# Performance work log

Measured on AMD Instinct MI355X. Metric: run time of the kernel, lower is better.

Reference implementation:

```python
import jax, jax.numpy as jnp
import numpy as np

L = 2048          # seq len
DIM = 1024        # model dim
NL = 12           # num layers
VOCAB = 50257
PAD_VOCAB = 50264 # vocab padded to multiple of 8 for embedding
N = 16            # ssm state dim
K = 4             # conv kernel size
E = 2048          # d_inner = expand * dim
DTR = 64          # dt_rank = ceil(dim/16)
EPS = 1e-5


def setup_inputs() -> dict:
    key = jax.random.key(0)
    ks = jax.random.split(key, 12)
    s = 0.02
    f32 = jnp.float32
    # HiPPO-style A init: A_log = log(1..N) broadcast over channels
    A_log = jnp.log(jnp.broadcast_to(jnp.arange(1, N + 1, dtype=f32), (NL, E, N)))
    return {
        "input_ids": jax.random.randint(ks[0], (L,), 0, VOCAB),
        "embed": jax.random.normal(ks[1], (PAD_VOCAB, DIM), f32) * s,
        "in_proj_w": jax.random.normal(ks[2], (NL, 2 * E, DIM), f32) * s,
        "conv_w": jax.random.normal(ks[3], (NL, E, K), f32) * s,
        "conv_b": jnp.zeros((NL, E), f32),
        "x_proj_w": jax.random.normal(ks[4], (NL, DTR + 2 * N, E), f32) * s,
        "dt_proj_w": jax.random.normal(ks[5], (NL, E, DTR), f32) * s,
        "dt_proj_b": jax.random.normal(ks[6], (NL, E), f32) * 0.1,
        "A_log": A_log,
        "D_param": jnp.ones((NL, E), f32),
        "out_proj_w": jax.random.normal(ks[7], (NL, DIM, E), f32) * s,
        "norm_w": jnp.ones((NL, DIM), f32),
        "norm_f_w": jnp.ones((DIM,), f32),
        "head_w": jax.random.normal(ks[8], (VOCAB, DIM), f32) * s,
    }


def rmsnorm(x, w):
    # per-token RMSNorm over last axis (matches eqx.nn.RMSNorm vmapped per token)
    inv = jax.lax.rsqrt(jnp.mean(x * x, axis=-1, keepdims=True) + EPS)
    return x * inv * w


def causal_dw_conv(x, w, b):
    # x: [L, E], w: [E, K] depthwise causal conv, b: [E]
    out = jax.lax.conv_general_dilated(
        x.T[None],            # [1, E, L]
        w[:, None, :],        # [E, 1, K]
        (1,), [(K - 1, 0)],
        feature_group_count=E,
        dimension_numbers=("NCH", "OIH", "NCH"),
    )
    return out[0].T + b       # [L, E]


def mamba_block(x, in_w, cw, cb, xp_w, dt_w, dt_b, A_log, D, out_w):
    # x: [L, DIM]
    xz = x @ in_w.T                       # [L, 2E]
    xi, z = xz[:, :E], xz[:, E:]
    xc = jax.nn.silu(causal_dw_conv(xi, cw, cb))   # [L, E]
    dbc = xc @ xp_w.T                     # [L, DTR + 2N]
    dt = jax.nn.softplus(dbc[:, :DTR] @ dt_w.T + dt_b)  # [L, E]
    B = dbc[:, DTR:DTR + N]               # [L, N]
    C = dbc[:, DTR + N:]                  # [L, N]
    A = -jnp.exp(A_log)                   # [E, N]
    dA = jnp.exp(dt[:, :, None] * A)                       # [L, E, N]
    dBu = dt[:, :, None] * B[:, None, :] * xc[:, :, None]  # [L, E, N]

    def step(h, inp):
        dA_t, dBu_t = inp
        h = dA_t * h + dBu_t
        return h, h

    _, hs = jax.lax.scan(step, jnp.zeros((E, N), x.dtype), (dA, dBu))
    y = jnp.einsum("len,ln->le", hs, C) + D * xc
    y = y * jax.nn.silu(z)
    return y @ out_w.T                    # [L, DIM]


def reference(input_ids, embed, in_proj_w, conv_w, conv_b, x_proj_w,
              dt_proj_w, dt_proj_b, A_log, D_param, out_proj_w,
              norm_w, norm_f_w, head_w):
    x = embed[input_ids]                  # [L, DIM]
    res = None
    for i in range(NL):
        res = x + res if res is not None else x
        h = rmsnorm(res, norm_w[i])
        x = mamba_block(h, in_proj_w[i], conv_w[i], conv_b[i], x_proj_w[i],
                        dt_proj_w[i], dt_proj_b[i], A_log[i], D_param[i],
                        out_proj_w[i])
    res = x + res
    x = rmsnorm(res, norm_f_w)
    return x @ head_w.T                   # [L, VOCAB]
```

## Files before the change

kernel.cpp:

```cpp
#include <hip/hip_runtime.h>
#include <math.h>

#define LSEQ 2048
#define DMODEL 1024
#define NLAYER 12
#define NVOCAB 50257
#define NPADV 50432
#define EDIM 2048
#define NST 16
#define DTRANK 64
#define EPSV 1e-5f
#define NCHUNK 64
#define TCHUNK 32

typedef __attribute__((ext_vector_type(4))) float float4v;
typedef __attribute__((ext_vector_type(8))) short short8v;
typedef __attribute__((ext_vector_type(4))) unsigned short ushort4v;
typedef unsigned short u16;

__device__ __forceinline__ u16 f2bf(float f) {
    union { float f; unsigned int u; } v; v.f = f;
    unsigned int r = v.u + 0x7FFFu + ((v.u >> 16) & 1u);
    return (u16)(r >> 16);
}

__device__ __forceinline__ ushort4v cvt4(float4 a) {
    ushort4v r; r[0] = f2bf(a.x); r[1] = f2bf(a.y); r[2] = f2bf(a.z); r[3] = f2bf(a.w);
    return r;
}

__device__ __forceinline__ short8v pack8(float4 a, float4 b) {
    short8v r;
    r[0] = (short)f2bf(a.x); r[1] = (short)f2bf(a.y); r[2] = (short)f2bf(a.z); r[3] = (short)f2bf(a.w);
    r[4] = (short)f2bf(b.x); r[5] = (short)f2bf(b.y); r[6] = (short)f2bf(b.z); r[7] = (short)f2bf(b.w);
    return r;
}

__device__ __forceinline__ float4v mfma_bf16(short8v a, short8v b, float4v c) {
    return __builtin_amdgcn_mfma_f32_16x16x32_bf16(a, b, c, 0, 0, 0);
}

__device__ __forceinline__ void gload_lds16(const void* g, void* l) {
    __builtin_amdgcn_global_load_lds(
        (const __attribute__((address_space(1))) unsigned int*)g,
        (__attribute__((address_space(3))) unsigned int*)l,
        16, 0, 0);
}

__global__ __launch_bounds__(256) void k_embed(const int* __restrict__ ids,
                                               const float* __restrict__ emb,
                                               float* __restrict__ res) {
    const int t = blockIdx.x;
    const int row = ids[t];
    ((float4*)(res + (size_t)t * DMODEL))[threadIdx.x] =
        ((const float4*)(emb + (size_t)row * DMODEL))[threadIdx.x];
}

template<bool ADD>
__global__ __launch_bounds__(256) void k_addnorm(float* __restrict__ res,
                                                 const float* __restrict__ xin,
                                                 const float* __restrict__ w,
                                                 u16* __restrict__ h) {
    const int t = blockIdx.x;
    const int i = threadIdx.x;
    float4 r = ((float4*)(res + (size_t)t * DMODEL))[i];
    if (ADD) {
        float4 xv = ((const float4*)(xin + (size_t)t * DMODEL))[i];
        r.x += xv.x; r.y += xv.y; r.z += xv.z; r.w += xv.w;
        ((float4*)(res + (size_t)t * DMODEL))[i] = r;
    }
    float ss = r.x * r.x + r.y * r.y + r.z * r.z + r.w * r.w;
#pragma unroll
    for (int off = 32; off > 0; off >>= 1) ss += __shfl_xor(ss, off);
    __shared__ float part[4];
    if ((i & 63) == 0) part[i >> 6] = ss;
    __syncthreads();
    float tot = part[0] + part[1] + part[2] + part[3];
    const float inv = rsqrtf(tot * (1.f / DMODEL) + EPSV);
    float4 wv = ((const float4*)w)[i];
    float4 o;
    o.x = r.x * inv * wv.x; o.y = r.y * inv * wv.y;
    o.z = r.z * inv * wv.z; o.w = r.w * inv * wv.w;
    ((ushort4v*)(h + (size_t)t * DMODEL))[i] = cvt4(o);
}

__global__ __launch_bounds__(256) void k_cvt(const float* __restrict__ s, u16* __restrict__ d,
                                             long long n, long long ntot) {
    const long long stride = (long long)gridDim.x * 256 * 8;
    for (long long i = ((long long)blockIdx.x * 256 + threadIdx.x) * 8; i < ntot; i += stride) {
        ushort4v lo, hi;
        if (i < n) {
            float4 a = *(const float4*)(s + i);
            float4 b = *(const float4*)(s + i + 4);
            lo = cvt4(a); hi = cvt4(b);
        } else {
            lo[0] = lo[1] = lo[2] = lo[3] = 0;
            hi[0] = hi[1] = hi[2] = hi[3] = 0;
        }
        *(ushort4v*)(d + i) = lo;
        *(ushort4v*)(d + i + 4) = hi;
    }
}

__global__ __launch_bounds__(256) void k_cvt2(const float* __restrict__ sa, u16* __restrict__ da, long long na,
                                              const float* __restrict__ sb, u16* __restrict__ db, long long nb) {
    const long long tot = na + nb;
    const long long stride = (long long)gridDim.x * 256 * 8;
    for (long long i = ((long long)blockIdx.x * 256 + threadIdx.x) * 8; i < tot; i += stride) {
        const float* s; u16* d; long long o;
        if (i < na) { s = sa; d = da; o = i; } else { s = sb; d = db; o = i - na; }
        float4 a = *(const float4*)(s + o);
        float4 b = *(const float4*)(s + o + 4);
        *(ushort4v*)(d + o) = cvt4(a);
        *(ushort4v*)(d + o + 4) = cvt4(b);
    }
}

template<int MT>
__global__ __launch_bounds__(512, 2) void k_gemm256(const u16* __restrict__ A,
                                                    const u16* __restrict__ W,
                                                    float* __restrict__ C,
                                                    int N, int K, int ldc, int cpx) {
    __shared__ __align__(128) u16 lds[2][2][2][8192];
    const int tid = threadIdx.x;
    const int w = tid >> 6;
    const int lane = tid & 63;
    const int l16 = lane & 15;
    const int quad = lane >> 4;
    const int wm = (w >> 2) * 128;
    const int wn = (w & 3) * 64;
    const int ha = w >> 2;
    const int hb = (w >> 1) & 1;
    const int bid = blockIdx.x;
    const int orig = (bid & 7) * cpx + (bid >> 3);
    const int bm = orig & (MT - 1);
    const int bn = orig / MT;
    const int row0 = bm * 256, col0 = bn * 256;

    int srow[2], scol[2];
#pragma unroll
    for (int q = 0; q < 2; ++q) {
        int off = q * 8192 + w * 1024 + lane * 16;
        off ^= ((off >> 7) & 7) << 4;
        srow[q] = off >> 7;
        scol[q] = (off & 127) >> 1;
    }
    const int qx0 = (quad * 16) ^ ((l16 & 7) << 4);
    const int bA0 = l16 * 128 + qx0;
    const int bA1 = bA0 ^ 64;
    const int bB0 = ((wn & 127) + l16) * 128 + qx0;
    const int bB1 = bB0 ^ 64;

    float4v acc[8][4];
#pragma unroll
    for (int i = 0; i < 8; ++i)
#pragma unroll
        for (int j = 0; j < 4; ++j)
#pragma unroll
            for (int r = 0; r < 4; ++r) acc[i][j][r] = 0.f;

    const int NT = K >> 6;

    auto stage_tile = [&](int buf, int t) {
#pragma unroll
        for (int h = 0; h < 2; ++h)
#pragma unroll
            for (int q = 0; q < 2; ++q) {
                gload_lds16(A + (size_t)(row0 + h * 128 + srow[q]) * K + t * 64 + scol[q],
                            &lds[buf][0][h][q * 4096 + w * 512]);
                gload_lds16(W + (size_t)(col0 + h * 128 + srow[q]) * K + t * 64 + scol[q],
                            &lds[buf][1][h][q * 4096 + w * 512]);
            }
    };

    stage_tile(0, 0);
    stage_tile(1, 1);
    asm volatile("s_waitcnt vmcnt(8)" ::: "memory");
    __builtin_amdgcn_s_barrier();

    for (int n = 0; n < NT; ++n) {
        const u16* As0 = &lds[n & 1][0][ha][0];
        const u16* Bs0 = &lds[n & 1][1][hb][0];
#pragma unroll
        for (int ph = 0; ph < 4; ++ph) {
            const int ih = ph & 1;
            const int ks = ph >> 1;
            const int bA = ks ? bA1 : bA0;
            const int bB = ks ? bB1 : bB0;
            short8v af[4], bf[4];
#pragma unroll
            for (int ii = 0; ii < 4; ++ii)
                af[ii] = *(const short8v*)((const char*)As0 + (bA + ih * 8192 + ii * 2048));
#pragma unroll
            for (int j = 0; j < 4; ++j)
                bf[j] = *(const short8v*)((const char*)Bs0 + (bB + j * 2048));
            __builtin_amdgcn_s_barrier();
            __builtin_amdgcn_s_setprio(1);
#pragma unroll
            for (int ii = 0; ii < 4; ++ii)
#pragma unroll
                for (int j = 0; j < 4; ++j)
                    acc[ih * 4 + ii][j] = mfma_bf16(af[ii], bf[j], acc[ih * 4 + ii][j]);
            __builtin_amdgcn_s_setprio(0);
            if (ph == 3) {
                if (n + 2 < NT) {
                    stage_tile(n & 1, n + 2);
                    asm volatile("s_waitcnt vmcnt(8)" ::: "memory");
                } else if (n < NT - 1) {
                    asm volatile("s_waitcnt vmcnt(0)" ::: "memory");
                }
            }
            __builtin_amdgcn_s_barrier();
        }
    }

#pragma unroll
    for (int i = 0; i < 8; ++i) {
        const int row = row0 + wm + i * 16 + quad * 4;
#pragma unroll
        for (int j = 0; j < 4; ++j) {
            const int col = col0 + wn + j * 16 + l16;
            if (col < N) {
#pragma unroll
                for (int r = 0; r < 4; ++r)
                    C[(size_t)(row + r) * ldc + col] = acc[i][j][r];
            }
        }
    }
}

template<int TM, int TN>
__global__ __launch_bounds__(256) void k_gemm_bf(const u16* __restrict__ A,
                                                 const u16* __restrict__ W,
                                                 float* __restrict__ C,
                                                 int N, int K, int ldc) {
    constexpr int NI = TM / 32, NJ = TN / 32, CA = TM / 64, CB = TN / 64;
    __shared__ u16 As[TM * 32];
    __shared__ u16 Bs[TN * 32];
    const int tid = threadIdx.x;
    const int lane = tid & 63;
    const int wave = tid >> 6;
    const int l16 = lane & 15;
    const int quad = lane >> 4;
    const int wm = (wave >> 1) * (TM / 2);
    const int wn = (wave & 1) * (TN / 2);
    const int srow = lane >> 2;
    const int scol = (((lane & 3) ^ ((lane >> 2) & 3))) * 8;
    const int bm = blockIdx.x, bn = blockIdx.y;

    const u16* Ab = A + ((size_t)bm * TM + srow) * K + scol;
    const u16* Wb = W + ((size_t)bn * TN + srow) * K + scol;

    const int qs = (quad ^ (l16 & 3)) * 8;

    float4v acc[NI][NJ];
#pragma unroll
    for (int i = 0; i < NI; ++i)
#pragma unroll
        for (int j = 0; j < NJ; ++j)
#pragma unroll
            for (int r = 0; r < 4; ++r) acc[i][j][r] = 0.f;

    for (int k0 = 0; k0 < K; k0 += 32) {
#pragma unroll
        for (int c = 0; c < CA; ++c) {
            const int chunk = wave * CA + c;
            gload_lds16(Ab + (size_t)chunk * 16 * K + k0, &As[chunk * 512]);
        }
#pragma unroll
        for (int c = 0; c < CB; ++c) {
            const int chunk = wave * CB + c;
            gload_lds16(Wb + (size_t)chunk * 16 * K + k0, &Bs[chunk * 512]);
        }
        __syncthreads();
        short8v af[NI], bfr[NJ];
#pragma unroll
        for (int i = 0; i < NI; ++i)
            af[i] = *(const short8v*)&As[(wm + i * 16 + l16) * 32 + qs];
#pragma unroll
        for (int j = 0; j < NJ; ++j)
            bfr[j] = *(const short8v*)&Bs[(wn + j * 16 + l16) * 32 + qs];
#pragma unroll
        for (int i = 0; i < NI; ++i)
#pragma unroll
            for (int j = 0; j < NJ; ++j)
                acc[i][j] = mfma_bf16(af[i], bfr[j], acc[i][j]);
        __syncthreads();
    }

#pragma unroll
    for (int i = 0; i < NI; ++i) {
        const int row0 = bm * TM + wm + i * 16 + quad * 4;
#pragma unroll
        for (int j = 0; j < NJ; ++j) {
            const int col = bn * TN + wn + j * 16 + l16;
            if (col < N) {
#pragma unroll
                for (int r = 0; r < 4; ++r)
                    C[(size_t)(row0 + r) * ldc + col] = acc[i][j][r];
            }
        }
    }
}

template<int EPI>
__global__ __launch_bounds__(256) void k_gemm(const float* __restrict__ A,
                                              const float* __restrict__ W,
                                              float* __restrict__ C,
                                              const float* __restrict__ bias,
                                              int N, int K, int lda, int ldw, int ldc) {
    __shared__ u16 As[128][32];
    __shared__ u16 Bs[128][32];
    const int tid = threadIdx.x;
    const int lane = tid & 63;
    const int wave = tid >> 6;
    const int l16 = lane & 15;
    const int quad = lane >> 4;
    const int wm = (wave >> 1) * 64;
    const int wn = (wave & 1) * 64;
    const int srow = tid >> 3;
    const int scol = (tid & 7) * 4;
    const int bm = blockIdx.x, bn = blockIdx.y;

    const float* Ap = A + (size_t)(bm * 128 + srow) * lda + scol;
    const int gn0 = bn * 128 + srow;

    float4 apf[4], bpf[4];
#pragma unroll
    for (int i = 0; i < 4; ++i) {
        apf[i] = *(const float4*)(Ap + (size_t)(32 * i) * lda);
        const int gn = gn0 + 32 * i;
        bpf[i] = (gn < N) ? *(const float4*)(W + (size_t)gn * ldw + scol)
                          : make_float4(0.f, 0.f, 0.f, 0.f);
    }

    float4v acc[4][4];
#pragma unroll
    for (int i = 0; i < 4; ++i)
#pragma unroll
        for (int j = 0; j < 4; ++j)
#pragma unroll
            for (int r = 0; r < 4; ++r) acc[i][j][r] = 0.f;

    int k0 = 0;
    while (true) {
#pragma unroll
        for (int i = 0; i < 4; ++i) {
            *(ushort4v*)&As[srow + 32 * i][scol] = cvt4(apf[i]);
            *(ushort4v*)&Bs[srow + 32 * i][scol] = cvt4(bpf[i]);
        }
        __syncthreads();
        k0 += 32;
        const bool more = (k0 < K);
        if (more) {
#pragma unroll
            for (int i = 0; i < 4; ++i) {
                apf[i] = *(const float4*)(Ap + (size_t)(32 * i) * lda + k0);
                const int gn = gn0 + 32 * i;
                bpf[i] = (gn < N) ? *(const float4*)(W + (size_t)gn * ldw + scol + k0)
                                  : make_float4(0.f, 0.f, 0.f, 0.f);
            }
        }
        short8v af[4], bfr[4];
#pragma unroll
        for (int i = 0; i < 4; ++i)
            af[i] = *(const short8v*)&As[wm + i * 16 + l16][quad * 8];
#pragma unroll
        for (int j = 0; j < 4; ++j)
            bfr[j] = *(const short8v*)&Bs[wn + j * 16 + l16][quad * 8];
#pragma unroll
        for (int i = 0; i < 4; ++i)
#pragma unroll
            for (int j = 0; j < 4; ++j)
                acc[i][j] = mfma_bf16(af[i], bfr[j], acc[i][j]);
        if (!more) break;
        __syncthreads();
    }

#pragma unroll
    for (int i = 0; i < 4; ++i) {
        const int row0 = bm * 128 + wm + i * 16 + quad * 4;
#pragma unroll
        for (int j = 0; j < 4; ++j) {
            const int col = bn * 128 + wn + j * 16 + l16;
            if (col < N) {
#pragma unroll
                for (int r = 0; r < 4; ++r) {
                    float v = acc[i][j][r];
                    if (EPI == 1) {
                        v += bias[col];
                        v = (v > 20.f) ? v : log1pf(__expf(v));
                    }
                    C[(size_t)(row0 + r) * ldc + col] = v;
                }
            }
        }
    }
}

__global__ __launch_bounds__(256) void k_conv(const float* __restrict__ xz,
                                              const float* __restrict__ cw,
                                              const float* __restrict__ cb,
                                              float* __restrict__ xc) {
    const int e = blockIdx.x * 256 + threadIdx.x;
    const int t0 = blockIdx.y * 8;
    const float w0 = cw[e * 4 + 0], w1 = cw[e * 4 + 1], w2 = cw[e * 4 + 2], w3 = cw[e * 4 + 3];
    const float b = cb[e];
    float xm3 = (t0 >= 3) ? xz[(size_t)(t0 - 3) * (2 * EDIM) + e] : 0.f;
    float xm2 = (t0 >= 2) ? xz[(size_t)(t0 - 2) * (2 * EDIM) + e] : 0.f;
    float xm1 = (t0 >= 1) ? xz[(size_t)(t0 - 1) * (2 * EDIM) + e] : 0.f;
#pragma unroll
    for (int s = 0; s < 8; ++s) {
        const int t = t0 + s;
        const float xt = xz[(size_t)t * (2 * EDIM) + e];
        const float v = w0 * xm3 + w1 * xm2 + w2 * xm1 + w3 * xt + b;
        xc[(size_t)t * EDIM + e] = v / (1.f + __expf(-v));
        xm3 = xm2; xm2 = xm1; xm1 = xt;
    }
}

__global__ __launch_bounds__(256) void k_xproj(const float* __restrict__ xc,
                                               const float* __restrict__ W,
                                               float* __restrict__ dbc) {
    const int tid = threadIdx.x;
    const int wave = tid >> 6, lane = tid & 63;
    const int l16 = lane & 15, quad = lane >> 4;
    const int m = blockIdx.x * 16 + l16;
    const int kb = wave * (EDIM / 4);
    float4v acc[6];
#pragma unroll
    for (int j = 0; j < 6; ++j)
#pragma unroll
        for (int r = 0; r < 4; ++r) acc[j][r] = 0.f;

    for (int ks = 0; ks < EDIM / 4; ks += 32) {
        const int k = kb + ks + quad * 8;
        const float* ap = xc + (size_t)m * EDIM + k;
        const short8v af = pack8(*(const float4*)ap, *(const float4*)(ap + 4));
#pragma unroll
        for (int j = 0; j < 6; ++j) {
            const float* wp = W + (size_t)(j * 16 + l16) * EDIM + k;
            const short8v bf = pack8(*(const float4*)wp, *(const float4*)(wp + 4));
            acc[j] = mfma_bf16(af, bf, acc[j]);
        }
    }
    __shared__ float red[4][16][96];
#pragma unroll
    for (int j = 0; j < 6; ++j)
#pragma unroll
        for (int r = 0; r < 4; ++r)
            red[wave][quad * 4 + r][j * 16 + l16] = acc[j][r];
    __syncthreads();
    for (int idx = tid; idx < 16 * 96; idx += 256) {
        const int r = idx / 96, c = idx % 96;
        const float s = red[0][r][c] + red[1][r][c] + red[2][r][c] + red[3][r][c];
        dbc[(size_t)(blockIdx.x * 16 + r) * 96 + c] = s;
    }
}

__global__ __launch_bounds__(256) void k_scanA(const float* __restrict__ dt,
                                               const float* __restrict__ xc,
                                               const float* __restrict__ dbc,
                                               const float* __restrict__ Al,
                                               float* __restrict__ hpart,
                                               float* __restrict__ sdtb) {
    const int e = blockIdx.y * 256 + threadIdx.x;
    const int c = blockIdx.x;
    float a[NST];
#pragma unroll
    for (int n = 0; n < NST; ++n) a[n] = -__expf(Al[(size_t)e * NST + n]);
    bool fast = true;
#pragma unroll
    for (int n = 0; n < NST; ++n)
        fast = fast && (fabsf(a[n] + (float)(n + 1)) < 1e-3f * (float)(n + 1));
    __align__(16) float h[NST];
#pragma unroll
    for (int n = 0; n < NST; ++n) h[n] = 0.f;
    float sdt = 0.f;
    const int t0 = c * TCHUNK;
    if (fast) {
        for (int s = 0; s < TCHUNK; ++s) {
            const int t = t0 + s;
            const float d = dt[(size_t)t * EDIM + e];
            const float x = xc[(size_t)t * EDIM + e];
            __align__(16) float Bv[NST];
#pragma unroll
            for (int q = 0; q < 4; ++q)
                *(float4*)&Bv[q * 4] = *(const float4*)&dbc[(size_t)t * 96 + 64 + q * 4];
            const float u = d * x;
            sdt += d;
            const float d1 = __expf(-d);
            float pw = 1.f;
#pragma unroll
            for (int n = 0; n < NST; ++n) { pw *= d1; h[n] = fmaf(pw, h[n], u * Bv[n]); }
        }
    } else {
        for (int s = 0; s < TCHUNK; ++s) {
            const int t = t0 + s;
            const float d = dt[(size_t)t * EDIM + e];
            const float x = xc[(size_t)t * EDIM + e];
            __align__(16) float Bv[NST];
#pragma unroll
            for (int q = 0; q < 4; ++q)
                *(float4*)&Bv[q * 4] = *(const float4*)&dbc[(size_t)t * 96 + 64 + q * 4];
            const float u = d * x;
            sdt += d;
#pragma unroll
            for (int n = 0; n < NST; ++n) h[n] = fmaf(__expf(d * a[n]), h[n], u * Bv[n]);
        }
    }
#pragma unroll
    for (int n = 0; n < NST; n += 4)
        *(float4*)&hpart[((size_t)c * EDIM + e) * NST + n] = *(float4*)&h[n];
    sdtb[(size_t)c * EDIM + e] = sdt;
}

__global__ __launch_bounds__(256) void k_scanB(float* __restrict__ hio,
                                               const float* __restrict__ sdtb,
                                               const float* __restrict__ Al) {
    const int idx = blockIdx.x * 256 + threadIdx.x;
    const int e = idx >> 4;
    const float a = -__expf(Al[idx]);
    float carry = 0.f;
    for (int c = 0; c < NCHUNK; ++c) {
        const size_t off = ((size_t)c * EDIM + e) * NST + (idx & 15);
        const float hp = hio[off];
        const float ap = __expf(a * sdtb[(size_t)c * EDIM + e]);
        hio[off] = carry;
        carry = fmaf(ap, carry, hp);
    }
}

__global__ __launch_bounds__(256) void k_scanC(const float* __restrict__ dt,
                                               const float* __restrict__ xc,
                                               const float* __restrict__ dbc,
                                               const float* __restrict__ xz,
                                               const float* __restrict__ Al,
                                               const float* __restrict__ Dl,
                                               const float* __restrict__ hin,
                                               u16* __restrict__ y) {
    const int e = blockIdx.y * 256 + threadIdx.x;
    const int c = blockIdx.x;
    float a[NST];
#pragma unroll
    for (int n = 0; n < NST; ++n) a[n] = -__expf(Al[(size_t)e * NST + n]);
    bool fast = true;
#pragma unroll
    for (int n = 0; n < NST; ++n)
        fast = fast && (fabsf(a[n] + (float)(n + 1)) < 1e-3f * (float)(n + 1));
    __align__(16) float h[NST];
#pragma unroll
    for (int n = 0; n < NST; n += 4)
        *(float4*)&h[n] = *(const float4*)&hin[((size_t)c * EDIM + e) * NST + n];
    const float Dv = Dl[e];
    const int t0 = c * TCHUNK;
    for (int s = 0; s < TCHUNK; ++s) {
        const int t = t0 + s;
        const float d = dt[(size_t)t * EDIM + e];
        const float x = xc[(size_t)t * EDIM + e];
        __align__(16) float Bv[NST], Cv[NST];
#pragma unroll
        for (int q = 0; q < 4; ++q) {
            *(float4*)&Bv[q * 4] = *(const float4*)&dbc[(size_t)t * 96 + 64 + q * 4];
            *(float4*)&Cv[q * 4] = *(const float4*)&dbc[(size_t)t * 96 + 80 + q * 4];
        }
        const float u = d * x;
        float ys = 0.f;
        if (fast) {
            const float d1 = __expf(-d);
            float pw = 1.f;
#pragma unroll
            for (int n = 0; n < NST; ++n) {
                pw *= d1;
                h[n] = fmaf(pw, h[n], u * Bv[n]);
                ys = fmaf(h[n], Cv[n], ys);
            }
        } else {
#pragma unroll
            for (int n = 0; n < NST; ++n) {
                h[n] = fmaf(__expf(d * a[n]), h[n], u * Bv[n]);
                ys = fmaf(h[n], Cv[n], ys);
            }
        }
        const float z = xz[(size_t)t * (2 * EDIM) + EDIM + e];
        const float yv = ys + Dv * x;
        y[(size_t)t * EDIM + e] = f2bf(yv * (z / (1.f + __expf(-z))));
    }
}

extern "C" void kernel_launch(void* const* d_in, const int* in_sizes, int n_in,
                              void* d_out, int out_size, void* d_ws, size_t ws_size,
                              hipStream_t stream) {
    const int*   ids   = (const int*)d_in[0];
    const float* emb   = (const float*)d_in[1];
    const float* inW   = (const float*)d_in[2];
    const float* convW = (const float*)d_in[3];
    const float* convB = (const float*)d_in[4];
    const float* xpW   = (const float*)d_in[5];
    const float* dtW   = (const float*)d_in[6];
    const float* dtB   = (const float*)d_in[7];
    const float* Alog  = (const float*)d_in[8];
    const float* Dpar  = (const float*)d_in[9];
    const float* outW  = (const float*)d_in[10];
    const float* normW = (const float*)d_in[11];
    const float* normF = (const float*)d_in[12];
    const float* headW = (const float*)d_in[13];
    float* out = (float*)d_out;

    float* ws    = (float*)d_ws;
    float* res   = ws;
    float* xzb   = res   + (size_t)LSEQ * DMODEL;
    float* xcb   = xzb   + (size_t)LSEQ * 2 * EDIM;
    float* dbcb  = xcb   + (size_t)LSEQ * EDIM;
    float* dtb   = dbcb  + (size_t)LSEQ * 96;
    float* xob   = dtb   + (size_t)LSEQ * EDIM;
    float* hpart = xob   + (size_t)LSEQ * DMODEL;
    float* sdtb  = hpart + (size_t)NCHUNK * EDIM * NST;
    u16* hbf  = (u16*)(sdtb + (size_t)NCHUNK * EDIM);
    u16* ybf  = hbf  + (size_t)LSEQ * DMODEL;
    u16* wbf  = ybf  + (size_t)LSEQ * EDIM;
    u16* wbf2 = wbf  + (size_t)2 * EDIM * DMODEL;

    k_embed<<<LSEQ, 256, 0, stream>>>(ids, emb, res);

    for (int i = 0; i < NLAYER; ++i) {
        if (i == 0)
            k_addnorm<false><<<LSEQ, 256, 0, stream>>>(res, nullptr, normW, hbf);
        else
            k_addnorm<true><<<LSEQ, 256, 0, stream>>>(res, xob, normW + (size_t)i * DMODEL, hbf);

        k_cvt2<<<4096, 256, 0, stream>>>(inW + (size_t)i * 2 * EDIM * DMODEL, wbf,
                                         (long long)2 * EDIM * DMODEL,
                                         outW + (size_t)i * DMODEL * EDIM, wbf2,
                                         (long long)DMODEL * EDIM);

        k_gemm256<8><<<dim3(128), 512, 0, stream>>>(hbf, wbf, xzb,
                2 * EDIM, DMODEL, 2 * EDIM, 16);

        k_conv<<<dim3(8, 256), 256, 0, stream>>>(xzb, convW + (size_t)i * EDIM * 4,
                convB + (size_t)i * EDIM, xcb);

        k_xproj<<<128, 256, 0, stream>>>(xcb, xpW + (size_t)i * 96 * EDIM, dbcb);

        k_gemm<1><<<dim3(16, 16), 256, 0, stream>>>(dbcb, dtW + (size_t)i * EDIM * DTRANK,
                dtb, dtB + (size_t)i * EDIM, EDIM, DTRANK, 96, DTRANK, EDIM);

        const float* Al = Alog + (size_t)i * EDIM * NST;
        k_scanA<<<dim3(NCHUNK, EDIM / 256), 256, 0, stream>>>(dtb, xcb, dbcb, Al, hpart, sdtb);
        k_scanB<<<(EDIM * NST) / 256, 256, 0, stream>>>(hpart, sdtb, Al);
        k_scanC<<<dim3(NCHUNK, EDIM / 256), 256, 0, stream>>>(dtb, xcb, dbcb, xzb, Al,
                Dpar + (size_t)i * EDIM, hpart, ybf);

        k_gemm_bf<64, 64><<<dim3(32, 16), 256, 0, stream>>>(ybf, wbf2, xob,
                DMODEL, EDIM, DMODEL);
    }

    k_addnorm<true><<<LSEQ, 256, 0, stream>>>(res, xob, normF, hbf);

    k_cvt<<<4096, 256, 0, stream>>>(headW, wbf,
            (long long)NVOCAB * DMODEL, (long long)NPADV * DMODEL);
    k_gemm256<8><<<dim3(8 * (NPADV / 256)), 512, 0, stream>>>(hbf, wbf, out,
            NVOCAB, DMODEL, NVOCAB, NPADV / 256);
}
```

Baseline: 3.302 ms.

## Replace 256x256 GEMM tile with 128x128 tile kernel and trim vocab padding

Replaces the 512-thread 256x256-tile bf16 MFMA GEMM with a 256-thread 128x128-tile kernel using K-step 32, a new LDS swizzle and double buffering, and targets 4 blocks per CU. It is used for both the in_proj GEMM (512 blocks instead of 128) and the vocab head GEMM. Vocab padding drops from 50432 to 50304, a multiple of 128, which reduces wasted head-GEMM tiles and the conversion work. The aim is better CU occupancy and load balance across the MI355X's many CUs. The cost is less data reuse per tile and more global and LDS traffic.

```diff
diff --git a/kernel.cpp b/kernel.cpp
--- a/kernel.cpp
+++ b/kernel.cpp
@@ -5,7 +5,7 @@
 #define DMODEL 1024
 #define NLAYER 12
 #define NVOCAB 50257
-#define NPADV 50432
+#define NPADV 50304
 #define EDIM 2048
 #define NST 16
 #define DTRANK 64
@@ -117,105 +117,87 @@
 }
 
 template<int MT>
-__global__ __launch_bounds__(512, 2) void k_gemm256(const u16* __restrict__ A,
+__global__ __launch_bounds__(256, 4) void k_gemm128(const u16* __restrict__ A,
                                                     const u16* __restrict__ W,
                                                     float* __restrict__ C,
                                                     int N, int K, int ldc, int cpx) {
-    __shared__ __align__(128) u16 lds[2][2][2][8192];
+    __shared__ __align__(128) u16 lds[2][8192];
     const int tid = threadIdx.x;
     const int w = tid >> 6;
     const int lane = tid & 63;
     const int l16 = lane & 15;
     const int quad = lane >> 4;
-    const int wm = (w >> 2) * 128;
-    const int wn = (w & 3) * 64;
-    const int ha = w >> 2;
-    const int hb = (w >> 1) & 1;
+    const int wm = (w >> 1) * 64;
+    const int wn = (w & 1) * 64;
     const int bid = blockIdx.x;
     const int orig = (bid & 7) * cpx + (bid >> 3);
     const int bm = orig & (MT - 1);
     const int bn = orig / MT;
-    const int row0 = bm * 256, col0 = bn * 256;
-
-    int srow[2], scol[2];
-#pragma unroll
-    for (int q = 0; q < 2; ++q) {
-        int off = q * 8192 + w * 1024 + lane * 16;
-        off ^= ((off >> 7) & 7) << 4;
-        srow[q] = off >> 7;
-        scol[q] = (off & 127) >> 1;
-    }
-    const int qx0 = (quad * 16) ^ ((l16 & 7) << 4);
-    const int bA0 = l16 * 128 + qx0;
-    const int bA1 = bA0 ^ 64;
-    const int bB0 = ((wn & 127) + l16) * 128 + qx0;
-    const int bB1 = bB0 ^ 64;
-
-    float4v acc[8][4];
-#pragma unroll
-    for (int i = 0; i < 8; ++i)
+    const int row0 = bm * 128, col0 = bn * 128;
+
+    const int scol = ((lane & 3) ^ ((lane >> 2) & 3)) * 8;
+    const int lrow = lane >> 2;
+    const u16* sbase[4];
+#pragma unroll
+    for (int c = 0; c < 4; ++c) {
+        const int g = w * 4 + c;
+        sbase[c] = (g < 8 ? A + (size_t)(row0 + g * 16 + lrow) * K
+                          : W + (size_t)(col0 + (g - 8) * 16 + lrow) * K) + scol;
+    }
+
+    const int swz = (quad ^ (l16 & 3)) * 8;
+    const int aoff = (wm + l16) * 32 + swz;
+    const int boff = 4096 + (wn + l16) * 32 + swz;
+
+    float4v acc[4][4];
+#pragma unroll
+    for (int i = 0; i < 4; ++i)
 #pragma unroll
         for (int j = 0; j < 4; ++j)
 #pragma unroll
             for (int r = 0; r < 4; ++r) acc[i][j][r] = 0.f;
 
-    const int NT = K >> 6;
+    const int NT = K >> 5;
 
     auto stage_tile = [&](int buf, int t) {
 #pragma unroll
-        for (int h = 0; h < 2; ++h)
-#pragma unroll
-            for (int q = 0; q < 2; ++q) {
-                gload_lds16(A + (size_t)(row0 + h * 128 + srow[q]) * K + t * 64 + scol[q],
-                            &lds[buf][0][h][q * 4096 + w * 512]);
-                gload_lds16(W + (size_t)(col0 + h * 128 + srow[q]) * K + t * 64 + scol[q],
-                            &lds[buf][1][h][q * 4096 + w * 512]);
-            }
+        for (int c = 0; c < 4; ++c)
+            gload_lds16(sbase[c] + t * 32, &lds[buf][(w * 4 + c) * 512]);
     };
 
     stage_tile(0, 0);
     stage_tile(1, 1);
-    asm volatile("s_waitcnt vmcnt(8)" ::: "memory");
+    asm volatile("s_waitcnt vmcnt(4)" ::: "memory");
     __builtin_amdgcn_s_barrier();
 
     for (int n = 0; n < NT; ++n) {
-        const u16* As0 = &lds[n & 1][0][ha][0];
-        const u16* Bs0 = &lds[n & 1][1][hb][0];
-#pragma unroll
-        for (int ph = 0; ph < 4; ++ph) {
-            const int ih = ph & 1;
-            const int ks = ph >> 1;
-            const int bA = ks ? bA1 : bA0;
-            const int bB = ks ? bB1 : bB0;
-            short8v af[4], bf[4];
-#pragma unroll
-            for (int ii = 0; ii < 4; ++ii)
-                af[ii] = *(const short8v*)((const char*)As0 + (bA + ih * 8192 + ii * 2048));
+        const u16* Ls = &lds[n & 1][0];
+        short8v af[4], bf[4];
+#pragma unroll
+        for (int ii = 0; ii < 4; ++ii)
+            af[ii] = *(const short8v*)&Ls[aoff + ii * 512];
+#pragma unroll
+        for (int j = 0; j < 4; ++j)
+            bf[j] = *(const short8v*)&Ls[boff + j * 512];
+        __builtin_amdgcn_s_barrier();
+        __builtin_amdgcn_s_setprio(1);
+#pragma unroll
+        for (int ii = 0; ii < 4; ++ii)
 #pragma unroll
             for (int j = 0; j < 4; ++j)
-                bf[j] = *(const short8v*)((const char*)Bs0 + (bB + j * 2048));
-            __builtin_amdgcn_s_barrier();
-            __builtin_amdgcn_s_setprio(1);
-#pragma unroll
-            for (int ii = 0; ii < 4; ++ii)
-#pragma unroll
-                for (int j = 0; j < 4; ++j)
-                    acc[ih * 4 + ii][j] = mfma_bf16(af[ii], bf[j], acc[ih * 4 + ii][j]);
-            __builtin_amdgcn_s_setprio(0);
-            if (ph == 3) {
-                if (n + 2 < NT) {
-                    stage_tile(n & 1, n + 2);
-                    asm volatile("s_waitcnt vmcnt(8)" ::: "memory");
-                } else if (n < NT - 1) {
-                    asm volatile("s_waitcnt vmcnt(0)" ::: "memory");
-                }
-            }
-            __builtin_amdgcn_s_barrier();
-        }
-    }
-
-#pragma unroll
-    for (int i = 0; i < 8; ++i) {
+                acc[ii][j] = mfma_bf16(af[ii], bf[j], acc[ii][j]);
+        __builtin_amdgcn_s_setprio(0);
+        if (n + 2 < NT) {
+            stage_tile(n & 1, n + 2);
+            asm volatile("s_waitcnt vmcnt(4)" ::: "memory");
+        } else if (n < NT - 1) {
+            asm volatile("s_waitcnt vmcnt(0)" ::: "memory");
+        }
+        __builtin_amdgcn_s_barrier();
+    }
+
+#pragma unroll
+    for (int i = 0; i < 4; ++i) {
         const int row = row0 + wm + i * 16 + quad * 4;
 #pragma unroll
         for (int j = 0; j < 4; ++j) {
@@ -634,8 +616,8 @@
                                          outW + (size_t)i * DMODEL * EDIM, wbf2,
                                          (long long)DMODEL * EDIM);
 
-        k_gemm256<8><<<dim3(128), 512, 0, stream>>>(hbf, wbf, xzb,
-                2 * EDIM, DMODEL, 2 * EDIM, 16);
+        k_gemm128<16><<<dim3(512), 256, 0, stream>>>(hbf, wbf, xzb,
+                2 * EDIM, DMODEL, 2 * EDIM, 64);
 
         k_conv<<<dim3(8, 256), 256, 0, stream>>>(xzb, convW + (size_t)i * EDIM * 4,
                 convB + (size_t)i * EDIM, xcb);
@@ -659,6 +641,6 @@
 
     k_cvt<<<4096, 256, 0, stream>>>(headW, wbf,
             (long long)NVOCAB * DMODEL, (long long)NPADV * DMODEL);
-    k_gemm256<8><<<dim3(8 * (NPADV / 256)), 512, 0, stream>>>(hbf, wbf, out,
-            NVOCAB, DMODEL, NVOCAB, NPADV / 256);
-}
+    k_gemm128<16><<<dim3(6288), 256, 0, stream>>>(hbf, wbf, out,
+            NVOCAB, DMODEL, NVOCAB, 6288 / 8);
+}
```

New measurement: 3.158 ms. 4.4% less time.
